# Optimization experiments

Hardware: AMD Instinct MI355X
Metric: run time of the kernel (lower is better)

The kernel has to match this reference:

```python
import jax, jax.numpy as jnp
import numpy as np

POOL = (2, 2)
B, H, W, C = 8, 128, 128, 256
FLAT_OUT = (H * POOL[0]) * (W * POOL[1]) * C  # 16,777,216


def setup_inputs() -> dict:
    key = jax.random.key(0)
    k1, k2 = jax.random.split(key)
    updates = jax.random.normal(k1, (B, H, W, C), dtype=jnp.float32)
    mask = jax.random.randint(k2, (B, H, W, C), 0, FLAT_OUT, dtype=jnp.int32)
    return {"updates": updates, "mask": mask}


def reference(updates, mask):
    ph, pw = POOL
    b, h, w, c = updates.shape
    hout, wout = h * ph, w * pw
    flat_input_size = h * w * c            # NOTE: original uses INPUT size as batch offset
    flat_output_size = hout * wout * c
    # per-batch offset (replicates b * flat_input_size from the TF code)
    batch_range = jnp.arange(b, dtype=jnp.int32).reshape(-1, 1, 1, 1)
    flat_mask = (mask.astype(jnp.int32) + batch_range * flat_input_size).reshape(-1)
    flat_updates = updates.reshape(-1)
    flat_output = jnp.zeros((b * flat_output_size,), dtype=updates.dtype)
    flat_output = flat_output.at[flat_mask].add(flat_updates)
    return flat_output.reshape(b, hout, wout, c)
```

## Files before the change

kernel.cpp:

```cpp
#include <hip/hip_runtime.h>


typedef float floatx4 __attribute__((ext_vector_type(4)));

constexpr int FLAT_IN   = 1 << 22;
constexpr int N_ELEMS   = 8 * FLAT_IN;
constexpr int OUT_WIN   = 7 * FLAT_IN + (1 << 24);
constexpr int OUT_TOTAL = 134217728;

constexpr int CB_SHIFT = 16;
constexpr int NBC      = OUT_WIN >> CB_SHIFT;
constexpr int NBC_PAD  = 768;

constexpr int AP_SHIFT = 15;
constexpr int APW      = 1 << AP_SHIFT;
constexpr int NAP      = OUT_TOTAL >> AP_SHIFT;
constexpr int NAP_WIN  = OUT_WIN >> AP_SHIFT;

constexpr int PBLOCK   = 1024;
constexpr int CHUNK    = 131072;
constexpr int NBLK     = N_ELEMS / CHUNK;
constexpr int ITERS    = CHUNK / (4 * PBLOCK);
constexpr int SEGS     = 8;
constexpr int SEG_ROWS = NBLK / SEGS;

constexpr size_t WS_PAIRS  = 0;
constexpr size_t WS_HISTC  = 268435456;
constexpr size_t WS_SEGC   = WS_HISTC + (size_t)NBLK * NBC_PAD * 4;
constexpr size_t WS_BBC    = WS_SEGC + (size_t)SEGS * NBC_PAD * 4;
constexpr size_t WS_NEEDED = WS_BBC + (size_t)(NBC_PAD + 1) * 4;

__global__ __launch_bounds__(256) void zero_kernel(floatx4* __restrict__ p, int n4) {
  int i = blockIdx.x * 256 + threadIdx.x;
  int stride = gridDim.x * 256;
  floatx4 z = {0.f, 0.f, 0.f, 0.f};
  for (; i < n4; i += stride) __builtin_nontemporal_store(z, p + i);
}

__global__ __launch_bounds__(PBLOCK) void p1_hist(const int4* __restrict__ mask4,
                                                  int* __restrict__ hist_c) {
  __shared__ int cnt[256];
  const int blk = blockIdx.x, tid = threadIdx.x;
  if (tid < 256) cnt[tid] = 0;
  __syncthreads();
  const int base4 = blk * (CHUNK / 4);
  #pragma unroll 4
  for (int k = 0; k < ITERS; ++k) {
    int4 m = mask4[base4 + k * PBLOCK + tid];
    atomicAdd(&cnt[m.x >> CB_SHIFT], 1);
    atomicAdd(&cnt[m.y >> CB_SHIFT], 1);
    atomicAdd(&cnt[m.z >> CB_SHIFT], 1);
    atomicAdd(&cnt[m.w >> CB_SHIFT], 1);
  }
  __syncthreads();
  const int cb0 = ((blk * CHUNK) & ~(FLAT_IN - 1)) >> CB_SHIFT;
  for (int j = tid; j < NBC_PAD; j += PBLOCK) {
    int jj = j - cb0;
    hist_c[blk * NBC_PAD + j] = (jj >= 0 && jj < 256) ? cnt[jj] : 0;
  }
}

__global__ __launch_bounds__(256) void p2_segsum(const int* __restrict__ hist,
                                                 int* __restrict__ segsum) {
  int b = blockIdx.x * 256 + threadIdx.x;
  int seg = blockIdx.y;
  const int* p = hist + (size_t)(seg * SEG_ROWS) * NBC_PAD + b;
  int s = 0;
  #pragma unroll 4
  for (int k = 0; k < SEG_ROWS; ++k) s += p[(size_t)k * NBC_PAD];
  segsum[seg * NBC_PAD + b] = s;
}

__global__ __launch_bounds__(256) void p2_scan_c(const int* __restrict__ segsum,
                                                 int* __restrict__ bbase) {
  __shared__ int tot[NBC_PAD];
  __shared__ int partial[256];
  const int t = threadIdx.x;
  for (int j = t; j < NBC_PAD; j += 256) {
    int s = 0;
    #pragma unroll
    for (int g = 0; g < SEGS; ++g) s += segsum[g * NBC_PAD + j];
    tot[j] = s;
  }
  __syncthreads();
  int local = 0;
  #pragma unroll
  for (int k = 0; k < NBC_PAD / 256; ++k) local += tot[t * (NBC_PAD / 256) + k];
  partial[t] = local;
  __syncthreads();
  for (int off = 1; off < 256; off <<= 1) {
    int tmp = (t >= off) ? partial[t - off] : 0;
    __syncthreads();
    partial[t] += tmp;
    __syncthreads();
  }
  int run = partial[t] - local;
  #pragma unroll
  for (int k = 0; k < NBC_PAD / 256; ++k) {
    int b = t * (NBC_PAD / 256) + k;
    bbase[b] = run;
    run += tot[b];
  }
  if (t == 255) bbase[NBC_PAD] = run;
}

__global__ __launch_bounds__(256) void p2_expand(int* __restrict__ hist,
                                                 const int* __restrict__ segsum) {
  int b = blockIdx.x * 256 + threadIdx.x;
  int seg = blockIdx.y;
  int run = 0;
  for (int g = 0; g < seg; ++g) run += segsum[g * NBC_PAD + b];
  int* p = hist + (size_t)(seg * SEG_ROWS) * NBC_PAD + b;
  for (int k = 0; k < SEG_ROWS; ++k) {
    int v = p[(size_t)k * NBC_PAD];
    p[(size_t)k * NBC_PAD] = run;
    run += v;
  }
}

__global__ __launch_bounds__(PBLOCK) void p3a_place(const int4* __restrict__ mask4,
                                                    const float4* __restrict__ upd4,
                                                    const int* __restrict__ hist_c,
                                                    const int* __restrict__ bbase_c,
                                                    int2* __restrict__ pout) {
  __shared__ int cnt[256];
  __shared__ int rowbase[256];
  const int blk = blockIdx.x, tid = threadIdx.x;
  const int boff = (blk * CHUNK) & ~(FLAT_IN - 1);
  const int cb0 = boff >> CB_SHIFT;
  if (tid < 256) {
    cnt[tid] = 0;
    rowbase[tid] = bbase_c[cb0 + tid] + hist_c[blk * NBC_PAD + cb0 + tid];
  }
  __syncthreads();
  const int base4 = blk * (CHUNK / 4);
  #pragma unroll 2
  for (int k = 0; k < ITERS; ++k) {
    int j4 = base4 + k * PBLOCK + tid;
    int4 m = mask4[j4];
    float4 u = upd4[j4];
    {
      int b = m.x >> CB_SHIFT; int r = atomicAdd(&cnt[b], 1);
      pout[rowbase[b] + r] = make_int2(m.x + boff, __float_as_int(u.x));
    }
    {
      int b = m.y >> CB_SHIFT; int r = atomicAdd(&cnt[b], 1);
      pout[rowbase[b] + r] = make_int2(m.y + boff, __float_as_int(u.y));
    }
    {
      int b = m.z >> CB_SHIFT; int r = atomicAdd(&cnt[b], 1);
      pout[rowbase[b] + r] = make_int2(m.z + boff, __float_as_int(u.z));
    }
    {
      int b = m.w >> CB_SHIFT; int r = atomicAdd(&cnt[b], 1);
      pout[rowbase[b] + r] = make_int2(m.w + boff, __float_as_int(u.w));
    }
  }
}

__global__ __launch_bounds__(1024) void p4c_apply(const int2* __restrict__ pairs,
                                                  const int* __restrict__ bbase,
                                                  float* __restrict__ out) {
  __shared__ float win[APW];
  const int tid = threadIdx.x;
  const int b = blockIdx.x;
  const int h = (b & ~15) | ((b & 7) << 1) | ((b >> 3) & 1);
  floatx4* w4 = (floatx4*)win;
  floatx4 z = {0.f, 0.f, 0.f, 0.f};
  #pragma unroll
  for (int k = 0; k < APW / 4096; ++k) w4[k * 1024 + tid] = z;
  if (h < NAP_WIN) {
    __syncthreads();
    const int cb = h >> 1;
    const int sel = h & 1;
    const int s = bbase[cb], e = bbase[cb + 1];
    const int s4 = (s + 1) & ~1;
    if ((s & 1) && s < e && tid == 0) {
      int2 p = pairs[s];
      if (((p.x >> AP_SHIFT) & 1) == sel)
        atomicAdd(&win[p.x & (APW - 1)], __int_as_float(p.y));
    }
    const int n2 = (e > s4) ? ((e - s4) >> 1) : 0;
    const int4* pv = (const int4*)(pairs + s4);
    for (int i = tid; i < n2; i += 1024) {
      int4 q = pv[i];
      if (((q.x >> AP_SHIFT) & 1) == sel)
        atomicAdd(&win[q.x & (APW - 1)], __int_as_float(q.y));
      if (((q.z >> AP_SHIFT) & 1) == sel)
        atomicAdd(&win[q.z & (APW - 1)], __int_as_float(q.w));
    }
    if ((e > s4) && ((e - s4) & 1) && tid == 0) {
      int2 p = pairs[e - 1];
      if (((p.x >> AP_SHIFT) & 1) == sel)
        atomicAdd(&win[p.x & (APW - 1)], __int_as_float(p.y));
    }
    __syncthreads();
  }
  floatx4* o4 = (floatx4*)(out + (size_t)h * APW);
  #pragma unroll
  for (int k = 0; k < APW / 4096; ++k)
    __builtin_nontemporal_store(w4[k * 1024 + tid], o4 + k * 1024 + tid);
}

__global__ __launch_bounds__(256) void scatter_add4_kernel(
    const float4* __restrict__ upd4, const int4* __restrict__ msk4,
    float* __restrict__ out, int n4) {
  int j = blockIdx.x * blockDim.x + threadIdx.x;
  if (j >= n4) return;
  float4 u = upd4[j];
  int4 m = msk4[j];
  int base = (j * 4) & ~(FLAT_IN - 1);
  unsafeAtomicAdd(out + (base + m.x), u.x);
  unsafeAtomicAdd(out + (base + m.y), u.y);
  unsafeAtomicAdd(out + (base + m.z), u.z);
  unsafeAtomicAdd(out + (base + m.w), u.w);
}

extern "C" void kernel_launch(void* const* d_in, const int* in_sizes, int n_in,
                              void* d_out, int out_size, void* d_ws, size_t ws_size,
                              hipStream_t stream) {
  const float* updates = (const float*)d_in[0];
  const int*   mask    = (const int*)d_in[1];
  float*       out     = (float*)d_out;
  const int n = in_sizes[0];

  const bool fast = (n == N_ELEMS) && (out_size == OUT_TOTAL) && (ws_size >= WS_NEEDED);

  if (!fast) {
    int n4z = out_size / 4;
    zero_kernel<<<(n4z + 2047) / 2048, 256, 0, stream>>>((floatx4*)d_out, n4z);
    int n4 = n / 4;
    scatter_add4_kernel<<<(n4 + 255) / 256, 256, 0, stream>>>(
        (const float4*)updates, (const int4*)mask, out, n4);
    return;
  }

  char* ws = (char*)d_ws;
  int2* pairs   = (int2*)(ws + WS_PAIRS);
  int*  hist_c  = (int*)(ws + WS_HISTC);
  int*  segsum  = (int*)(ws + WS_SEGC);
  int*  bbase_c = (int*)(ws + WS_BBC);

  p1_hist<<<NBLK, PBLOCK, 0, stream>>>((const int4*)mask, hist_c);
  p2_segsum<<<dim3(NBC_PAD / 256, SEGS), 256, 0, stream>>>(hist_c, segsum);
  p2_scan_c<<<1, 256, 0, stream>>>(segsum, bbase_c);
  p2_expand<<<dim3(NBC_PAD / 256, SEGS), 256, 0, stream>>>(hist_c, segsum);
  p3a_place<<<NBLK, PBLOCK, 0, stream>>>((const int4*)mask, (const float4*)updates,
                                         hist_c, bbase_c, pairs);
  p4c_apply<<<NAP, 1024, 0, stream>>>(pairs, bbase_c, out);
}
```

Before: 1.109 ms.

## Align bucket width to apply window so each pair is read once

```diff
diff --git a/kernel.cpp b/kernel.cpp
--- a/kernel.cpp
+++ b/kernel.cpp
@@ -2,20 +2,21 @@
 
 
 typedef float floatx4 __attribute__((ext_vector_type(4)));
+typedef int   intx4   __attribute__((ext_vector_type(4)));
 
 constexpr int FLAT_IN   = 1 << 22;
 constexpr int N_ELEMS   = 8 * FLAT_IN;
 constexpr int OUT_WIN   = 7 * FLAT_IN + (1 << 24);
 constexpr int OUT_TOTAL = 134217728;
 
-constexpr int CB_SHIFT = 16;
+constexpr int CB_SHIFT = 15;
 constexpr int NBC      = OUT_WIN >> CB_SHIFT;
-constexpr int NBC_PAD  = 768;
-
-constexpr int AP_SHIFT = 15;
-constexpr int APW      = 1 << AP_SHIFT;
-constexpr int NAP      = OUT_TOTAL >> AP_SHIFT;
-constexpr int NAP_WIN  = OUT_WIN >> AP_SHIFT;
+constexpr int NBC_PAD  = 1536;
+constexpr int WIN_B    = 512;
+
+constexpr int APW      = 1 << CB_SHIFT;
+constexpr int NAP      = OUT_TOTAL >> CB_SHIFT;
+constexpr int NAP_WIN  = NBC;
 
 constexpr int PBLOCK   = 1024;
 constexpr int CHUNK    = 131072;
@@ -37,16 +38,16 @@
   for (; i < n4; i += stride) __builtin_nontemporal_store(z, p + i);
 }
 
-__global__ __launch_bounds__(PBLOCK) void p1_hist(const int4* __restrict__ mask4,
+__global__ __launch_bounds__(PBLOCK) void p1_hist(const intx4* __restrict__ mask4,
                                                   int* __restrict__ hist_c) {
-  __shared__ int cnt[256];
+  __shared__ int cnt[WIN_B];
   const int blk = blockIdx.x, tid = threadIdx.x;
-  if (tid < 256) cnt[tid] = 0;
+  if (tid < WIN_B) cnt[tid] = 0;
   __syncthreads();
   const int base4 = blk * (CHUNK / 4);
   #pragma unroll 4
   for (int k = 0; k < ITERS; ++k) {
-    int4 m = mask4[base4 + k * PBLOCK + tid];
+    intx4 m = mask4[base4 + k * PBLOCK + tid];
     atomicAdd(&cnt[m.x >> CB_SHIFT], 1);
     atomicAdd(&cnt[m.y >> CB_SHIFT], 1);
     atomicAdd(&cnt[m.z >> CB_SHIFT], 1);
@@ -56,7 +57,7 @@
   const int cb0 = ((blk * CHUNK) & ~(FLAT_IN - 1)) >> CB_SHIFT;
   for (int j = tid; j < NBC_PAD; j += PBLOCK) {
     int jj = j - cb0;
-    hist_c[blk * NBC_PAD + j] = (jj >= 0 && jj < 256) ? cnt[jj] : 0;
+    hist_c[blk * NBC_PAD + j] = (jj >= 0 && jj < WIN_B) ? cnt[jj] : 0;
   }
 }
 
@@ -118,17 +119,17 @@
   }
 }
 
-__global__ __launch_bounds__(PBLOCK) void p3a_place(const int4* __restrict__ mask4,
-                                                    const float4* __restrict__ upd4,
+__global__ __launch_bounds__(PBLOCK) void p3a_place(const intx4* __restrict__ mask4,
+                                                    const floatx4* __restrict__ upd4,
                                                     const int* __restrict__ hist_c,
                                                     const int* __restrict__ bbase_c,
                                                     int2* __restrict__ pout) {
-  __shared__ int cnt[256];
-  __shared__ int rowbase[256];
+  __shared__ int cnt[WIN_B];
+  __shared__ int rowbase[WIN_B];
   const int blk = blockIdx.x, tid = threadIdx.x;
   const int boff = (blk * CHUNK) & ~(FLAT_IN - 1);
   const int cb0 = boff >> CB_SHIFT;
-  if (tid < 256) {
+  if (tid < WIN_B) {
     cnt[tid] = 0;
     rowbase[tid] = bbase_c[cb0 + tid] + hist_c[blk * NBC_PAD + cb0 + tid];
   }
@@ -137,8 +138,8 @@
   #pragma unroll 2
   for (int k = 0; k < ITERS; ++k) {
     int j4 = base4 + k * PBLOCK + tid;
-    int4 m = mask4[j4];
-    float4 u = upd4[j4];
+    intx4 m = __builtin_nontemporal_load(mask4 + j4);
+    floatx4 u = __builtin_nontemporal_load(upd4 + j4);
     {
       int b = m.x >> CB_SHIFT; int r = atomicAdd(&cnt[b], 1);
       pout[rowbase[b] + r] = make_int2(m.x + boff, __float_as_int(u.x));
@@ -163,36 +164,29 @@
                                                   float* __restrict__ out) {
   __shared__ float win[APW];
   const int tid = threadIdx.x;
-  const int b = blockIdx.x;
-  const int h = (b & ~15) | ((b & 7) << 1) | ((b >> 3) & 1);
+  const int h = blockIdx.x;
   floatx4* w4 = (floatx4*)win;
   floatx4 z = {0.f, 0.f, 0.f, 0.f};
   #pragma unroll
   for (int k = 0; k < APW / 4096; ++k) w4[k * 1024 + tid] = z;
   if (h < NAP_WIN) {
     __syncthreads();
-    const int cb = h >> 1;
-    const int sel = h & 1;
-    const int s = bbase[cb], e = bbase[cb + 1];
+    const int s = bbase[h], e = bbase[h + 1];
     const int s4 = (s + 1) & ~1;
     if ((s & 1) && s < e && tid == 0) {
       int2 p = pairs[s];
-      if (((p.x >> AP_SHIFT) & 1) == sel)
-        atomicAdd(&win[p.x & (APW - 1)], __int_as_float(p.y));
+      atomicAdd(&win[p.x & (APW - 1)], __int_as_float(p.y));
     }
     const int n2 = (e > s4) ? ((e - s4) >> 1) : 0;
-    const int4* pv = (const int4*)(pairs + s4);
+    const intx4* pv = (const intx4*)(pairs + s4);
     for (int i = tid; i < n2; i += 1024) {
-      int4 q = pv[i];
-      if (((q.x >> AP_SHIFT) & 1) == sel)
-        atomicAdd(&win[q.x & (APW - 1)], __int_as_float(q.y));
-      if (((q.z >> AP_SHIFT) & 1) == sel)
-        atomicAdd(&win[q.z & (APW - 1)], __int_as_float(q.w));
+      intx4 q = __builtin_nontemporal_load(pv + i);
+      atomicAdd(&win[q.x & (APW - 1)], __int_as_float(q.y));
+      atomicAdd(&win[q.z & (APW - 1)], __int_as_float(q.w));
     }
     if ((e > s4) && ((e - s4) & 1) && tid == 0) {
       int2 p = pairs[e - 1];
-      if (((p.x >> AP_SHIFT) & 1) == sel)
-        atomicAdd(&win[p.x & (APW - 1)], __int_as_float(p.y));
+      atomicAdd(&win[p.x & (APW - 1)], __int_as_float(p.y));
     }
     __syncthreads();
   }
@@ -241,11 +235,11 @@
   int*  segsum  = (int*)(ws + WS_SEGC);
   int*  bbase_c = (int*)(ws + WS_BBC);
 
-  p1_hist<<<NBLK, PBLOCK, 0, stream>>>((const int4*)mask, hist_c);
+  p1_hist<<<NBLK, PBLOCK, 0, stream>>>((const intx4*)mask, hist_c);
   p2_segsum<<<dim3(NBC_PAD / 256, SEGS), 256, 0, stream>>>(hist_c, segsum);
   p2_scan_c<<<1, 256, 0, stream>>>(segsum, bbase_c);
   p2_expand<<<dim3(NBC_PAD / 256, SEGS), 256, 0, stream>>>(hist_c, segsum);
-  p3a_place<<<NBLK, PBLOCK, 0, stream>>>((const int4*)mask, (const float4*)updates,
+  p3a_place<<<NBLK, PBLOCK, 0, stream>>>((const intx4*)mask, (const floatx4*)updates,
                                          hist_c, bbase_c, pairs);
   p4c_apply<<<NAP, 1024, 0, stream>>>(pairs, bbase_c, out);
 }
```

Result: slower. 1.133 ms (+2.2%).
